# Kernel tuning notes

Measured on AMD Instinct MI355X. Metric: run time of the kernel, lower is better.

Reference implementation:

```python
import jax, jax.numpy as jnp
import numpy as np

B, H, S = 64, 1024, 512
MIN_VAL, MAX_VAL = -1.0, 1.0
EPS = 1e-8  # torch F.cosine_similarity default eps


def setup_inputs() -> dict:
    key = jax.random.key(0)
    k1, k2, k3 = jax.random.split(key, 3)
    tree_state = jax.random.normal(k1, (B, H), dtype=jnp.float32)
    seq_states = jax.random.normal(k2, (B, H, S), dtype=jnp.float32)
    # binary validity mask (float, as it is multiplied in)
    seq_mask = (jax.random.uniform(k3, (B, S)) < 0.9).astype(jnp.float32)
    return {"tree_state": tree_state, "seq_states": seq_states, "seq_mask": seq_mask}


def reference(tree_state, seq_states, seq_mask):
    # scan over the seq axis; carry h: (B, H)
    xs = (jnp.transpose(seq_states, (2, 0, 1)), seq_mask.T)  # (S,B,H), (S,B)

    def step(h, x):
        s, m = x  # s: (B,H), m: (B,)
        dot = jnp.sum(h * s, axis=-1)  # (B,)
        denom = jnp.maximum(
            jnp.linalg.norm(h, axis=-1) * jnp.linalg.norm(s, axis=-1), EPS
        )
        cos = (dot / denom)[:, None]  # (B,1)
        h_new = jnp.clip(h + (s - h * cos) * m[:, None], MIN_VAL, MAX_VAL)
        return h_new, None

    h, _ = jax.lax.scan(step, tree_state, xs)
    return h
```

## Files before the change

### kernel.cpp

```cpp
#include <hip/hip_runtime.h>


#define NB 64
#define NH 1024
#define NS 512

typedef float v4f __attribute__((ext_vector_type(4)));
typedef float v2f __attribute__((ext_vector_type(2)));

template <int N> struct ic { static constexpr int value = N; };

template <int CTRL>
__device__ __forceinline__ float dpp_add(float x) {
  int s = __builtin_amdgcn_update_dpp(0, __builtin_bit_cast(int, x), CTRL, 0xf,
                                      0xf, true);
  return x + __builtin_bit_cast(float, s);
}

__device__ __forceinline__ float readlane_f(float v, int lane) {
  return __builtin_bit_cast(
      float, __builtin_amdgcn_readlane(__builtin_bit_cast(int, v), lane));
}

__device__ __forceinline__ void wave_red3(float& a, float& b, float& c) {
  a = dpp_add<0x111>(a); b = dpp_add<0x111>(b); c = dpp_add<0x111>(c);
  a = dpp_add<0x112>(a); b = dpp_add<0x112>(b); c = dpp_add<0x112>(c);
  a = dpp_add<0x114>(a); b = dpp_add<0x114>(b); c = dpp_add<0x114>(c);
  a = dpp_add<0x118>(a); b = dpp_add<0x118>(b); c = dpp_add<0x118>(c);
  a = dpp_add<0x142>(a); b = dpp_add<0x142>(b); c = dpp_add<0x142>(c);
  a = dpp_add<0x143>(a); b = dpp_add<0x143>(b); c = dpp_add<0x143>(c);
  a = readlane_f(a, 63);
  b = readlane_f(b, 63);
  c = readlane_f(c, 63);
}

#define GLD4(dst, p) \
  asm volatile("global_load_dwordx4 %0, %1, off" : "=v"(dst) : "v"(p))
#define GLD1(dst, p) \
  asm volatile("global_load_dword %0, %1, off" : "=v"(dst) : "v"(p))

template <int IMM>
__device__ __forceinline__ void dsr128(v4f& d, unsigned a) {
  asm volatile("ds_read_b128 %[d], %[a] offset:%[o]"
               : [d] "=v"(d)
               : [a] "v"(a), [o] "n"(IMM));
}
template <int IMM>
__device__ __forceinline__ void dsw32(unsigned a, float v) {
  asm volatile("ds_write_b32 %[a], %[v] offset:%[o]" ::[a] "v"(a), [v] "v"(v),
               [o] "n"(IMM));
}

__device__ __forceinline__ v2f pk_fma(v2f a, v2f b, v2f c) {
  v2f d;
  asm("v_pk_fma_f32 %0, %1, %2, %3" : "=v"(d) : "v"(a), "v"(b), "v"(c));
  return d;
}
__device__ __forceinline__ v2f pk_mul(v2f a, v2f b) {
  v2f d;
  asm("v_pk_mul_f32 %0, %1, %2" : "=v"(d) : "v"(a), "v"(b));
  return d;
}
__device__ __forceinline__ v2f pk_add(v2f a, v2f b) {
  v2f d;
  asm("v_pk_add_f32 %0, %1, %2" : "=v"(d) : "v"(a), "v"(b));
  return d;
}

#define LGK0SV(s0, s1, s2, s3)                                       \
  asm volatile("s_waitcnt lgkmcnt(0)"                                \
               : "+v"(s0), "+v"(s1), "+v"(s2), "+v"(s3))

__global__ __launch_bounds__(256, 1) void otsu_scan_kernel(
    const float* __restrict__ tree,
    const float* __restrict__ seq,
    const float* __restrict__ mask,
    float* __restrict__ out) {
  __shared__ float lds[2 * 16 * 1024];
  const int b = blockIdx.x;
  const int tid = threadIdx.x;
  const int w = tid >> 6;
  const int l = tid & 63;
  const unsigned lb = (unsigned)(unsigned long long)(&lds[0]);

  if (w == 0) {
    const float* hrow = tree + b * NH + 4 * l;
    v4f hv0, hv1, hv2, hv3;
    GLD4(hv0, hrow);
    asm volatile("global_load_dwordx4 %0, %1, off offset:1024"
                 : "=v"(hv1) : "v"(hrow));
    asm volatile("global_load_dwordx4 %0, %1, off offset:2048"
                 : "=v"(hv2) : "v"(hrow));
    asm volatile("global_load_dwordx4 %0, %1, off offset:3072"
                 : "=v"(hv3) : "v"(hrow));
    float m8[8];
    {
      const float* mp = mask + b * NS + l;
      GLD1(m8[0], mp);
      GLD1(m8[1], mp + 64);
      GLD1(m8[2], mp + 128);
      GLD1(m8[3], mp + 192);
      GLD1(m8[4], mp + 256);
      GLD1(m8[5], mp + 320);
      GLD1(m8[6], mp + 384);
      GLD1(m8[7], mp + 448);
    }
    asm volatile("s_waitcnt vmcnt(0)"
                 : "+v"(hv0), "+v"(hv1), "+v"(hv2), "+v"(hv3), "+v"(m8[0]),
                   "+v"(m8[1]), "+v"(m8[2]), "+v"(m8[3]), "+v"(m8[4]),
                   "+v"(m8[5]), "+v"(m8[6]), "+v"(m8[7]));

    v2f h2[8];
    h2[0] = v2f{hv0[0], hv0[1]}; h2[1] = v2f{hv0[2], hv0[3]};
    h2[2] = v2f{hv1[0], hv1[1]}; h2[3] = v2f{hv1[2], hv1[3]};
    h2[4] = v2f{hv2[0], hv2[1]}; h2[5] = v2f{hv2[2], hv2[3]};
    h2[6] = v2f{hv3[0], hv3[1]}; h2[7] = v2f{hv3[2], hv3[3]};

    unsigned mbits = 0u;
#pragma unroll
    for (int i = 0; i < 8; ++i)
      if (m8[i] != 0.0f) mbits |= (1u << i);

    if (!(__builtin_amdgcn_readlane((int)mbits, 0) & 1)) {
#pragma unroll
      for (int p = 0; p < 8; ++p) {
        h2[p].x = __builtin_amdgcn_fmed3f(h2[p].x, -1.0f, 1.0f);
        h2[p].y = __builtin_amdgcn_fmed3f(h2[p].y, -1.0f, 1.0f);
      }
    }

    unsigned rb = lb + 16u * (unsigned)l;
    v4f sval[2][4];

    asm volatile("s_barrier" ::: "memory");

#pragma unroll 1
    for (int g = 0; g < 32; ++g) {
      const int lbase = (16 * g) & 63;
      const int msh = g >> 2;
      dsr128<0 * 4096 + 0>(sval[0][0], rb);
      dsr128<0 * 4096 + 1024>(sval[0][1], rb);
      dsr128<0 * 4096 + 2048>(sval[0][2], rb);
      dsr128<0 * 4096 + 3072>(sval[0][3], rb);
      auto step = [&](auto sc) {
        constexpr int T = decltype(sc)::value;
        LGK0SV(sval[T & 1][0], sval[T & 1][1], sval[T & 1][2],
               sval[T & 1][3]);
        if constexpr (T < 15) {
          dsr128<(T + 1) * 4096 + 0>(sval[(T + 1) & 1][0], rb);
          dsr128<(T + 1) * 4096 + 1024>(sval[(T + 1) & 1][1], rb);
          dsr128<(T + 1) * 4096 + 2048>(sval[(T + 1) & 1][2], rb);
          dsr128<(T + 1) * 4096 + 3072>(sval[(T + 1) & 1][3], rb);
        }
        const unsigned mw =
            (unsigned)__builtin_amdgcn_readlane((int)mbits, lbase + T);
        if ((mw >> msh) & 1u) {
          const v4f s0 = sval[T & 1][0], s1 = sval[T & 1][1],
                    s2 = sval[T & 1][2], s3 = sval[T & 1][3];
          v2f sp[8];
          sp[0] = v2f{s0[0], s0[1]}; sp[1] = v2f{s0[2], s0[3]};
          sp[2] = v2f{s1[0], s1[1]}; sp[3] = v2f{s1[2], s1[3]};
          sp[4] = v2f{s2[0], s2[1]}; sp[5] = v2f{s2[2], s2[3]};
          sp[6] = v2f{s3[0], s3[1]}; sp[7] = v2f{s3[2], s3[3]};
          v2f a0 = pk_mul(h2[0], sp[0]), a1 = pk_mul(h2[1], sp[1]);
          v2f a2 = pk_mul(h2[2], sp[2]), a3 = pk_mul(h2[3], sp[3]);
          v2f b0 = pk_mul(h2[0], h2[0]), b1 = pk_mul(h2[1], h2[1]);
          v2f b2 = pk_mul(h2[2], h2[2]), b3 = pk_mul(h2[3], h2[3]);
          v2f c0 = pk_mul(sp[0], sp[0]), c1 = pk_mul(sp[1], sp[1]);
          v2f c2 = pk_mul(sp[2], sp[2]), c3 = pk_mul(sp[3], sp[3]);
          a0 = pk_fma(h2[4], sp[4], a0); a1 = pk_fma(h2[5], sp[5], a1);
          a2 = pk_fma(h2[6], sp[6], a2); a3 = pk_fma(h2[7], sp[7], a3);
          b0 = pk_fma(h2[4], h2[4], b0); b1 = pk_fma(h2[5], h2[5], b1);
          b2 = pk_fma(h2[6], h2[6], b2); b3 = pk_fma(h2[7], h2[7], b3);
          c0 = pk_fma(sp[4], sp[4], c0); c1 = pk_fma(sp[5], sp[5], c1);
          c2 = pk_fma(sp[6], sp[6], c2); c3 = pk_fma(sp[7], sp[7], c3);
          v2f A = pk_add(pk_add(a0, a1), pk_add(a2, a3));
          v2f Bv = pk_add(pk_add(b0, b1), pk_add(b2, b3));
          v2f C = pk_add(pk_add(c0, c1), pk_add(c2, c3));
          float pd = A.x + A.y, ph = Bv.x + Bv.y, ps = C.x + C.y;
          wave_red3(pd, ph, ps);
          const float p = fmaxf(ph * ps, 1e-16f);
          const float cc = pd * __builtin_amdgcn_rsqf(p);
          const float aa = 1.0f - cc;
          const v2f av = v2f{aa, aa};
#pragma unroll
          for (int q = 0; q < 8; ++q) {
            v2f t = pk_fma(h2[q], av, sp[q]);
            h2[q].x = __builtin_amdgcn_fmed3f(t.x, -1.0f, 1.0f);
            h2[q].y = __builtin_amdgcn_fmed3f(t.y, -1.0f, 1.0f);
          }
        }
      };
      step(ic<0>{});  step(ic<1>{});  step(ic<2>{});  step(ic<3>{});
      step(ic<4>{});  step(ic<5>{});  step(ic<6>{});  step(ic<7>{});
      step(ic<8>{});  step(ic<9>{});  step(ic<10>{}); step(ic<11>{});
      step(ic<12>{}); step(ic<13>{}); step(ic<14>{}); step(ic<15>{});
      rb ^= 0x10000u;
      asm volatile("s_barrier" ::: "memory");
    }

    asm volatile("s_waitcnt vmcnt(0) lgkmcnt(0)" ::: "memory");
    float* orow = out + b * NH + 4 * l;
#pragma unroll
    for (int m = 0; m < 4; ++m) {
      float4 v;
      v.x = h2[2 * m].x;
      v.y = h2[2 * m].y;
      v.z = h2[2 * m + 1].x;
      v.w = h2[2 * m + 1].y;
      *(float4*)(orow + 256 * m) = v;
    }
  } else {
    const float* pbase = seq + (size_t)b * NH * NS + (l >> 2) * 512 +
                         (l & 3) * 4;
    const unsigned wpb =
        lb + 16384u * (unsigned)(l & 3) + 4u * (unsigned)(l >> 2);
    const int cb = w - 1;

    v4f ring[22];
#define STAGE(T_, BSEL_)                                                  \
    do {                                                                  \
      _Pragma("unroll") for (int k = 0; k < 22; ++k) {                    \
        const int c = 3 * k + cb;                                         \
        if (c < 64) {                                                     \
          const float* p_ = pbase + c * 8192 + (T_) * 16;                 \
          GLD4(ring[k], p_);                                              \
        }                                                                 \
      }                                                                   \
      asm volatile("s_waitcnt vmcnt(0)" ::: "memory");                    \
      _Pragma("unroll") for (int k = 0; k < 22; ++k) {                    \
        const int c = 3 * k + cb;                                         \
        if (c < 64) {                                                     \
          const unsigned a_ = wpb + (BSEL_) + 64u * (unsigned)c;          \
          dsw32<0>(a_, ring[k][0]);                                       \
          dsw32<4096>(a_, ring[k][1]);                                    \
          dsw32<8192>(a_, ring[k][2]);                                    \
          dsw32<12288>(a_, ring[k][3]);                                   \
        }                                                                 \
      }                                                                   \
      asm volatile("s_waitcnt lgkmcnt(0)" ::: "memory");                  \
    } while (0)

    STAGE(0, 0u);
    asm volatile("s_barrier" ::: "memory");

#pragma unroll 1
    for (int g = 0; g < 32; ++g) {
      if (g < 31) {
        const unsigned bsel = (unsigned)((g + 1) & 1) << 16;
        STAGE(g + 1, bsel);
      }
      asm volatile("s_barrier" ::: "memory");
    }
#undef STAGE
  }
}

extern "C" void kernel_launch(void* const* d_in, const int* in_sizes, int n_in,
                              void* d_out, int out_size, void* d_ws,
                              size_t ws_size, hipStream_t stream) {
  const float* tree = (const float*)d_in[0];
  const float* seq = (const float*)d_in[1];
  const float* mask = (const float*)d_in[2];
  float* out = (float*)d_out;
  otsu_scan_kernel<<<dim3(NB), dim3(256), 0, stream>>>(tree, seq, mask, out);
}
```

Before: 270.4 us.

## Pad LDS rows and deepen consumer LDS read prefetch to two steps

Pads each time-step row in LDS from 1024 to 1028 floats so the producer waves' strided 32-bit writes no longer all hit the same banks. The consumer wave now keeps three register buffers and issues LDS reads two steps ahead, waiting with lgkmcnt(4) instead of draining to zero. This hides more of the LDS read latency behind the serial per-step dot/norm/update chain. In exchange it uses more VGPRs and slightly more LDS, and relies on a finer-grained wait count being correct.

```diff
diff --git a/kernel.cpp b/kernel.cpp
--- a/kernel.cpp
+++ b/kernel.cpp
@@ -4,6 +4,9 @@
 #define NB 64
 #define NH 1024
 #define NS 512
+
+#define STRF 1028
+#define BUFF (16 * STRF)
 
 typedef float v4f __attribute__((ext_vector_type(4)));
 typedef float v2f __attribute__((ext_vector_type(2)));
@@ -67,16 +70,21 @@
   return d;
 }
 
-#define LGK0SV(s0, s1, s2, s3)                                       \
-  asm volatile("s_waitcnt lgkmcnt(0)"                                \
-               : "+v"(s0), "+v"(s1), "+v"(s2), "+v"(s3))
+#define LGK4SV(sv)                                                    \
+  asm volatile("s_waitcnt lgkmcnt(4)"                                 \
+               : "+v"((sv)[0]), "+v"((sv)[1]), "+v"((sv)[2]),         \
+                 "+v"((sv)[3]))
+#define LGK0SV(sv)                                                    \
+  asm volatile("s_waitcnt lgkmcnt(0)"                                 \
+               : "+v"((sv)[0]), "+v"((sv)[1]), "+v"((sv)[2]),         \
+                 "+v"((sv)[3]))
 
 __global__ __launch_bounds__(256, 1) void otsu_scan_kernel(
     const float* __restrict__ tree,
     const float* __restrict__ seq,
     const float* __restrict__ mask,
     float* __restrict__ out) {
-  __shared__ float lds[2 * 16 * 1024];
+  __shared__ float lds[2 * BUFF];
   const int b = blockIdx.x;
   const int tid = threadIdx.x;
   const int w = tid >> 6;
@@ -129,8 +137,8 @@
       }
     }
 
-    unsigned rb = lb + 16u * (unsigned)l;
-    v4f sval[2][4];
+    const unsigned rb0 = lb + 16u * (unsigned)l;
+    v4f sval[3][4];
 
     asm volatile("s_barrier" ::: "memory");
 
@@ -138,25 +146,33 @@
     for (int g = 0; g < 32; ++g) {
       const int lbase = (16 * g) & 63;
       const int msh = g >> 2;
-      dsr128<0 * 4096 + 0>(sval[0][0], rb);
-      dsr128<0 * 4096 + 1024>(sval[0][1], rb);
-      dsr128<0 * 4096 + 2048>(sval[0][2], rb);
-      dsr128<0 * 4096 + 3072>(sval[0][3], rb);
+      const unsigned rbuf = rb0 + ((g & 1) ? (unsigned)(BUFF * 4) : 0u);
+
+      dsr128<0 * 4112 + 0>(sval[0][0], rbuf);
+      dsr128<0 * 4112 + 1024>(sval[0][1], rbuf);
+      dsr128<0 * 4112 + 2048>(sval[0][2], rbuf);
+      dsr128<0 * 4112 + 3072>(sval[0][3], rbuf);
+      dsr128<1 * 4112 + 0>(sval[1][0], rbuf);
+      dsr128<1 * 4112 + 1024>(sval[1][1], rbuf);
+      dsr128<1 * 4112 + 2048>(sval[1][2], rbuf);
+      dsr128<1 * 4112 + 3072>(sval[1][3], rbuf);
+      LGK4SV(sval[0]);
+
       auto step = [&](auto sc) {
         constexpr int T = decltype(sc)::value;
-        LGK0SV(sval[T & 1][0], sval[T & 1][1], sval[T & 1][2],
-               sval[T & 1][3]);
-        if constexpr (T < 15) {
-          dsr128<(T + 1) * 4096 + 0>(sval[(T + 1) & 1][0], rb);
-          dsr128<(T + 1) * 4096 + 1024>(sval[(T + 1) & 1][1], rb);
-          dsr128<(T + 1) * 4096 + 2048>(sval[(T + 1) & 1][2], rb);
-          dsr128<(T + 1) * 4096 + 3072>(sval[(T + 1) & 1][3], rb);
+        if constexpr (T >= 1 && T <= 14) LGK4SV(sval[T % 3]);
+        else if constexpr (T == 15) LGK0SV(sval[0]);
+        if constexpr (T <= 13) {
+          dsr128<(T + 2) * 4112 + 0>(sval[(T + 2) % 3][0], rbuf);
+          dsr128<(T + 2) * 4112 + 1024>(sval[(T + 2) % 3][1], rbuf);
+          dsr128<(T + 2) * 4112 + 2048>(sval[(T + 2) % 3][2], rbuf);
+          dsr128<(T + 2) * 4112 + 3072>(sval[(T + 2) % 3][3], rbuf);
         }
         const unsigned mw =
             (unsigned)__builtin_amdgcn_readlane((int)mbits, lbase + T);
         if ((mw >> msh) & 1u) {
-          const v4f s0 = sval[T & 1][0], s1 = sval[T & 1][1],
-                    s2 = sval[T & 1][2], s3 = sval[T & 1][3];
+          const v4f s0 = sval[T % 3][0], s1 = sval[T % 3][1],
+                    s2 = sval[T % 3][2], s3 = sval[T % 3][3];
           v2f sp[8];
           sp[0] = v2f{s0[0], s0[1]}; sp[1] = v2f{s0[2], s0[3]};
           sp[2] = v2f{s1[0], s1[1]}; sp[3] = v2f{s1[2], s1[3]};
@@ -195,7 +211,6 @@
       step(ic<4>{});  step(ic<5>{});  step(ic<6>{});  step(ic<7>{});
       step(ic<8>{});  step(ic<9>{});  step(ic<10>{}); step(ic<11>{});
       step(ic<12>{}); step(ic<13>{}); step(ic<14>{}); step(ic<15>{});
-      rb ^= 0x10000u;
       asm volatile("s_barrier" ::: "memory");
     }
 
@@ -214,7 +229,7 @@
     const float* pbase = seq + (size_t)b * NH * NS + (l >> 2) * 512 +
                          (l & 3) * 4;
     const unsigned wpb =
-        lb + 16384u * (unsigned)(l & 3) + 4u * (unsigned)(l >> 2);
+        lb + 16448u * (unsigned)(l & 3) + 4u * (unsigned)(l >> 2);
     const int cb = w - 1;
 
     v4f ring[22];
@@ -232,10 +247,10 @@
         const int c = 3 * k + cb;                                         \
         if (c < 64) {                                                     \
           const unsigned a_ = wpb + (BSEL_) + 64u * (unsigned)c;          \
-          dsw32<0>(a_, ring[k][0]);                                       \
-          dsw32<4096>(a_, ring[k][1]);                                    \
-          dsw32<8192>(a_, ring[k][2]);                                    \
-          dsw32<12288>(a_, ring[k][3]);                                   \
+          dsw32<0 * 4112>(a_, ring[k][0]);                                \
+          dsw32<1 * 4112>(a_, ring[k][1]);                                \
+          dsw32<2 * 4112>(a_, ring[k][2]);                                \
+          dsw32<3 * 4112>(a_, ring[k][3]);                                \
         }                                                                 \
       }                                                                   \
       asm volatile("s_waitcnt lgkmcnt(0)" ::: "memory");                  \
@@ -247,7 +262,7 @@
 #pragma unroll 1
     for (int g = 0; g < 32; ++g) {
       if (g < 31) {
-        const unsigned bsel = (unsigned)((g + 1) & 1) << 16;
+        const unsigned bsel = ((g + 1) & 1) ? (unsigned)(BUFF * 4) : 0u;
         STAGE(g + 1, bsel);
       }
       asm volatile("s_barrier" ::: "memory");
```

New measurement: 266.0 us. About the same (-1.6%).

## Process two batch rows per block to interleave independent scan chains

Applied to the files above, without the earlier changes.

Each block now handles two batch rows with 32 blocks instead of 64. The compute wave runs both recurrences side by side, merging their wave reductions into one six-value DPP reduction, so one chain's latency can hide behind the other's. The LDS stage is re-laid out with a padded stride of 4112 bytes, which changes bank mapping, and holds 8 steps per stage over 64 rounds instead of 16 steps over 32. The cost is half as many CUs in use, twice the load traffic per block, and compute that is no longer skipped for masked steps.

```diff
diff --git a/kernel.cpp b/kernel.cpp
--- a/kernel.cpp
+++ b/kernel.cpp
@@ -1,9 +1,12 @@
 #include <hip/hip_runtime.h>
 
 
-#define NB 64
+#define NB 32
 #define NH 1024
 #define NS 512
+
+#define STRB 4112u
+#define BUFB 32896u
 
 typedef float v4f __attribute__((ext_vector_type(4)));
 typedef float v2f __attribute__((ext_vector_type(2)));
@@ -22,20 +25,29 @@
       float, __builtin_amdgcn_readlane(__builtin_bit_cast(int, v), lane));
 }
 
-__device__ __forceinline__ void wave_red3(float& a, float& b, float& c) {
+__device__ __forceinline__ void wave_red6(float& a, float& b, float& c,
+                                          float& d, float& e, float& f) {
   a = dpp_add<0x111>(a); b = dpp_add<0x111>(b); c = dpp_add<0x111>(c);
+  d = dpp_add<0x111>(d); e = dpp_add<0x111>(e); f = dpp_add<0x111>(f);
   a = dpp_add<0x112>(a); b = dpp_add<0x112>(b); c = dpp_add<0x112>(c);
+  d = dpp_add<0x112>(d); e = dpp_add<0x112>(e); f = dpp_add<0x112>(f);
   a = dpp_add<0x114>(a); b = dpp_add<0x114>(b); c = dpp_add<0x114>(c);
+  d = dpp_add<0x114>(d); e = dpp_add<0x114>(e); f = dpp_add<0x114>(f);
   a = dpp_add<0x118>(a); b = dpp_add<0x118>(b); c = dpp_add<0x118>(c);
+  d = dpp_add<0x118>(d); e = dpp_add<0x118>(e); f = dpp_add<0x118>(f);
   a = dpp_add<0x142>(a); b = dpp_add<0x142>(b); c = dpp_add<0x142>(c);
+  d = dpp_add<0x142>(d); e = dpp_add<0x142>(e); f = dpp_add<0x142>(f);
   a = dpp_add<0x143>(a); b = dpp_add<0x143>(b); c = dpp_add<0x143>(c);
-  a = readlane_f(a, 63);
-  b = readlane_f(b, 63);
-  c = readlane_f(c, 63);
+  d = dpp_add<0x143>(d); e = dpp_add<0x143>(e); f = dpp_add<0x143>(f);
+  a = readlane_f(a, 63); b = readlane_f(b, 63); c = readlane_f(c, 63);
+  d = readlane_f(d, 63); e = readlane_f(e, 63); f = readlane_f(f, 63);
 }
 
 #define GLD4(dst, p) \
   asm volatile("global_load_dwordx4 %0, %1, off" : "=v"(dst) : "v"(p))
+#define GLD4O(dst, p, OFF) \
+  asm volatile("global_load_dwordx4 %0, %1, off offset:" OFF \
+               : "=v"(dst) : "v"(p))
 #define GLD1(dst, p) \
   asm volatile("global_load_dword %0, %1, off" : "=v"(dst) : "v"(p))
 
@@ -67,188 +79,261 @@
   return d;
 }
 
-#define LGK0SV(s0, s1, s2, s3)                                       \
-  asm volatile("s_waitcnt lgkmcnt(0)"                                \
-               : "+v"(s0), "+v"(s1), "+v"(s2), "+v"(s3))
+template <int T>
+__device__ __forceinline__ void read_step(unsigned rb, v4f (&sv)[4]) {
+  dsr128<(int)(T * STRB) + 0>(sv[0], rb);
+  dsr128<(int)(T * STRB) + 1024>(sv[1], rb);
+  dsr128<(int)(T * STRB) + 2048>(sv[2], rb);
+  dsr128<(int)(T * STRB) + 3072>(sv[3], rb);
+}
+
+#define LGK0AB(a, b)                                                   \
+  asm volatile("s_waitcnt lgkmcnt(0)"                                  \
+               : "+v"((a)[0]), "+v"((a)[1]), "+v"((a)[2]),             \
+                 "+v"((a)[3]), "+v"((b)[0]), "+v"((b)[1]),             \
+                 "+v"((b)[2]), "+v"((b)[3]))
 
 __global__ __launch_bounds__(256, 1) void otsu_scan_kernel(
     const float* __restrict__ tree,
     const float* __restrict__ seq,
     const float* __restrict__ mask,
     float* __restrict__ out) {
-  __shared__ float lds[2 * 16 * 1024];
-  const int b = blockIdx.x;
+  __shared__ float lds[4 * 8 * 1028];
   const int tid = threadIdx.x;
   const int w = tid >> 6;
   const int l = tid & 63;
+  const int bA = 2 * blockIdx.x;
+  const int bB = bA + 1;
   const unsigned lb = (unsigned)(unsigned long long)(&lds[0]);
 
   if (w == 0) {
-    const float* hrow = tree + b * NH + 4 * l;
-    v4f hv0, hv1, hv2, hv3;
-    GLD4(hv0, hrow);
-    asm volatile("global_load_dwordx4 %0, %1, off offset:1024"
-                 : "=v"(hv1) : "v"(hrow));
-    asm volatile("global_load_dwordx4 %0, %1, off offset:2048"
-                 : "=v"(hv2) : "v"(hrow));
-    asm volatile("global_load_dwordx4 %0, %1, off offset:3072"
-                 : "=v"(hv3) : "v"(hrow));
-    float m8[8];
+    const float* hrA = tree + bA * NH + 4 * l;
+    const float* hrB = tree + bB * NH + 4 * l;
+    v4f hA0, hA1, hA2v, hA3, hB0, hB1, hB2v, hB3;
+    GLD4(hA0, hrA);
+    GLD4O(hA1, hrA, "1024");
+    GLD4O(hA2v, hrA, "2048");
+    GLD4O(hA3, hrA, "3072");
+    GLD4(hB0, hrB);
+    GLD4O(hB1, hrB, "1024");
+    GLD4O(hB2v, hrB, "2048");
+    GLD4O(hB3, hrB, "3072");
+    float mA[8], mB[8];
     {
-      const float* mp = mask + b * NS + l;
-      GLD1(m8[0], mp);
-      GLD1(m8[1], mp + 64);
-      GLD1(m8[2], mp + 128);
-      GLD1(m8[3], mp + 192);
-      GLD1(m8[4], mp + 256);
-      GLD1(m8[5], mp + 320);
-      GLD1(m8[6], mp + 384);
-      GLD1(m8[7], mp + 448);
+      const float* mpA = mask + bA * NS + l;
+      const float* mpB = mask + bB * NS + l;
+#pragma unroll
+      for (int i = 0; i < 8; ++i) GLD1(mA[i], mpA + 64 * i);
+#pragma unroll
+      for (int i = 0; i < 8; ++i) GLD1(mB[i], mpB + 64 * i);
     }
     asm volatile("s_waitcnt vmcnt(0)"
-                 : "+v"(hv0), "+v"(hv1), "+v"(hv2), "+v"(hv3), "+v"(m8[0]),
-                   "+v"(m8[1]), "+v"(m8[2]), "+v"(m8[3]), "+v"(m8[4]),
-                   "+v"(m8[5]), "+v"(m8[6]), "+v"(m8[7]));
-
-    v2f h2[8];
-    h2[0] = v2f{hv0[0], hv0[1]}; h2[1] = v2f{hv0[2], hv0[3]};
-    h2[2] = v2f{hv1[0], hv1[1]}; h2[3] = v2f{hv1[2], hv1[3]};
-    h2[4] = v2f{hv2[0], hv2[1]}; h2[5] = v2f{hv2[2], hv2[3]};
-    h2[6] = v2f{hv3[0], hv3[1]}; h2[7] = v2f{hv3[2], hv3[3]};
-
-    unsigned mbits = 0u;
-#pragma unroll
-    for (int i = 0; i < 8; ++i)
-      if (m8[i] != 0.0f) mbits |= (1u << i);
-
-    if (!(__builtin_amdgcn_readlane((int)mbits, 0) & 1)) {
+                 : "+v"(hA0), "+v"(hA1), "+v"(hA2v), "+v"(hA3), "+v"(hB0),
+                   "+v"(hB1), "+v"(hB2v), "+v"(hB3));
+    asm volatile("s_waitcnt vmcnt(0)"
+                 : "+v"(mA[0]), "+v"(mA[1]), "+v"(mA[2]), "+v"(mA[3]),
+                   "+v"(mA[4]), "+v"(mA[5]), "+v"(mA[6]), "+v"(mA[7]),
+                   "+v"(mB[0]), "+v"(mB[1]), "+v"(mB[2]), "+v"(mB[3]),
+                   "+v"(mB[4]), "+v"(mB[5]), "+v"(mB[6]), "+v"(mB[7]));
+
+    v2f hA[8], hB[8];
+    hA[0] = v2f{hA0[0], hA0[1]}; hA[1] = v2f{hA0[2], hA0[3]};
+    hA[2] = v2f{hA1[0], hA1[1]}; hA[3] = v2f{hA1[2], hA1[3]};
+    hA[4] = v2f{hA2v[0], hA2v[1]}; hA[5] = v2f{hA2v[2], hA2v[3]};
+    hA[6] = v2f{hA3[0], hA3[1]}; hA[7] = v2f{hA3[2], hA3[3]};
+    hB[0] = v2f{hB0[0], hB0[1]}; hB[1] = v2f{hB0[2], hB0[3]};
+    hB[2] = v2f{hB1[0], hB1[1]}; hB[3] = v2f{hB1[2], hB1[3]};
+    hB[4] = v2f{hB2v[0], hB2v[1]}; hB[5] = v2f{hB2v[2], hB2v[3]};
+    hB[6] = v2f{hB3[0], hB3[1]}; hB[7] = v2f{hB3[2], hB3[3]};
+
+    unsigned mbitsA = 0u, mbitsB = 0u;
+#pragma unroll
+    for (int i = 0; i < 8; ++i) {
+      if (mA[i] != 0.0f) mbitsA |= (1u << i);
+      if (mB[i] != 0.0f) mbitsB |= (1u << i);
+    }
+
+    if (!(__builtin_amdgcn_readlane((int)mbitsA, 0) & 1)) {
 #pragma unroll
       for (int p = 0; p < 8; ++p) {
-        h2[p].x = __builtin_amdgcn_fmed3f(h2[p].x, -1.0f, 1.0f);
-        h2[p].y = __builtin_amdgcn_fmed3f(h2[p].y, -1.0f, 1.0f);
+        hA[p].x = __builtin_amdgcn_fmed3f(hA[p].x, -1.0f, 1.0f);
+        hA[p].y = __builtin_amdgcn_fmed3f(hA[p].y, -1.0f, 1.0f);
       }
     }
-
-    unsigned rb = lb + 16u * (unsigned)l;
-    v4f sval[2][4];
+    if (!(__builtin_amdgcn_readlane((int)mbitsB, 0) & 1)) {
+#pragma unroll
+      for (int p = 0; p < 8; ++p) {
+        hB[p].x = __builtin_amdgcn_fmed3f(hB[p].x, -1.0f, 1.0f);
+        hB[p].y = __builtin_amdgcn_fmed3f(hB[p].y, -1.0f, 1.0f);
+      }
+    }
+
+    const unsigned rbA0 = lb + 16u * (unsigned)l;
+    const unsigned rbB0 = rbA0 + 2u * BUFB;
+    v4f svA[2][4], svB[2][4];
 
     asm volatile("s_barrier" ::: "memory");
 
 #pragma unroll 1
-    for (int g = 0; g < 32; ++g) {
-      const int lbase = (16 * g) & 63;
-      const int msh = g >> 2;
-      dsr128<0 * 4096 + 0>(sval[0][0], rb);
-      dsr128<0 * 4096 + 1024>(sval[0][1], rb);
-      dsr128<0 * 4096 + 2048>(sval[0][2], rb);
-      dsr128<0 * 4096 + 3072>(sval[0][3], rb);
+    for (int g = 0; g < 64; ++g) {
+      const int lbase = 8 * (g & 7);
+      const int msh = g >> 3;
+      const unsigned po = (g & 1) ? BUFB : 0u;
+      const unsigned rbA = rbA0 + po;
+      const unsigned rbB = rbB0 + po;
+
+      read_step<0>(rbA, svA[0]);
+      read_step<0>(rbB, svB[0]);
+
       auto step = [&](auto sc) {
         constexpr int T = decltype(sc)::value;
-        LGK0SV(sval[T & 1][0], sval[T & 1][1], sval[T & 1][2],
-               sval[T & 1][3]);
-        if constexpr (T < 15) {
-          dsr128<(T + 1) * 4096 + 0>(sval[(T + 1) & 1][0], rb);
-          dsr128<(T + 1) * 4096 + 1024>(sval[(T + 1) & 1][1], rb);
-          dsr128<(T + 1) * 4096 + 2048>(sval[(T + 1) & 1][2], rb);
-          dsr128<(T + 1) * 4096 + 3072>(sval[(T + 1) & 1][3], rb);
+        LGK0AB(svA[T & 1], svB[T & 1]);
+        if constexpr (T < 7) {
+          read_step<T + 1>(rbA, svA[(T + 1) & 1]);
+          read_step<T + 1>(rbB, svB[(T + 1) & 1]);
         }
-        const unsigned mw =
-            (unsigned)__builtin_amdgcn_readlane((int)mbits, lbase + T);
-        if ((mw >> msh) & 1u) {
-          const v4f s0 = sval[T & 1][0], s1 = sval[T & 1][1],
-                    s2 = sval[T & 1][2], s3 = sval[T & 1][3];
-          v2f sp[8];
-          sp[0] = v2f{s0[0], s0[1]}; sp[1] = v2f{s0[2], s0[3]};
-          sp[2] = v2f{s1[0], s1[1]}; sp[3] = v2f{s1[2], s1[3]};
-          sp[4] = v2f{s2[0], s2[1]}; sp[5] = v2f{s2[2], s2[3]};
-          sp[6] = v2f{s3[0], s3[1]}; sp[7] = v2f{s3[2], s3[3]};
-          v2f a0 = pk_mul(h2[0], sp[0]), a1 = pk_mul(h2[1], sp[1]);
-          v2f a2 = pk_mul(h2[2], sp[2]), a3 = pk_mul(h2[3], sp[3]);
-          v2f b0 = pk_mul(h2[0], h2[0]), b1 = pk_mul(h2[1], h2[1]);
-          v2f b2 = pk_mul(h2[2], h2[2]), b3 = pk_mul(h2[3], h2[3]);
-          v2f c0 = pk_mul(sp[0], sp[0]), c1 = pk_mul(sp[1], sp[1]);
-          v2f c2 = pk_mul(sp[2], sp[2]), c3 = pk_mul(sp[3], sp[3]);
-          a0 = pk_fma(h2[4], sp[4], a0); a1 = pk_fma(h2[5], sp[5], a1);
-          a2 = pk_fma(h2[6], sp[6], a2); a3 = pk_fma(h2[7], sp[7], a3);
-          b0 = pk_fma(h2[4], h2[4], b0); b1 = pk_fma(h2[5], h2[5], b1);
-          b2 = pk_fma(h2[6], h2[6], b2); b3 = pk_fma(h2[7], h2[7], b3);
-          c0 = pk_fma(sp[4], sp[4], c0); c1 = pk_fma(sp[5], sp[5], c1);
-          c2 = pk_fma(sp[6], sp[6], c2); c3 = pk_fma(sp[7], sp[7], c3);
-          v2f A = pk_add(pk_add(a0, a1), pk_add(a2, a3));
-          v2f Bv = pk_add(pk_add(b0, b1), pk_add(b2, b3));
-          v2f C = pk_add(pk_add(c0, c1), pk_add(c2, c3));
-          float pd = A.x + A.y, ph = Bv.x + Bv.y, ps = C.x + C.y;
-          wave_red3(pd, ph, ps);
-          const float p = fmaxf(ph * ps, 1e-16f);
-          const float cc = pd * __builtin_amdgcn_rsqf(p);
-          const float aa = 1.0f - cc;
-          const v2f av = v2f{aa, aa};
+        const v4f a0 = svA[T & 1][0], a1 = svA[T & 1][1],
+                  a2 = svA[T & 1][2], a3 = svA[T & 1][3];
+        const v4f b0 = svB[T & 1][0], b1 = svB[T & 1][1],
+                  b2 = svB[T & 1][2], b3 = svB[T & 1][3];
+        v2f sa[8], sb[8];
+        sa[0] = v2f{a0[0], a0[1]}; sa[1] = v2f{a0[2], a0[3]};
+        sa[2] = v2f{a1[0], a1[1]}; sa[3] = v2f{a1[2], a1[3]};
+        sa[4] = v2f{a2[0], a2[1]}; sa[5] = v2f{a2[2], a2[3]};
+        sa[6] = v2f{a3[0], a3[1]}; sa[7] = v2f{a3[2], a3[3]};
+        sb[0] = v2f{b0[0], b0[1]}; sb[1] = v2f{b0[2], b0[3]};
+        sb[2] = v2f{b1[0], b1[1]}; sb[3] = v2f{b1[2], b1[3]};
+        sb[4] = v2f{b2[0], b2[1]}; sb[5] = v2f{b2[2], b2[3]};
+        sb[6] = v2f{b3[0], b3[1]}; sb[7] = v2f{b3[2], b3[3]};
+        v2f dA0 = pk_mul(hA[0], sa[0]), dB0 = pk_mul(hB[0], sb[0]);
+        v2f dA1 = pk_mul(hA[1], sa[1]), dB1 = pk_mul(hB[1], sb[1]);
+        v2f dA2 = pk_mul(hA[2], sa[2]), dB2 = pk_mul(hB[2], sb[2]);
+        v2f dA3 = pk_mul(hA[3], sa[3]), dB3 = pk_mul(hB[3], sb[3]);
+        v2f eA0 = pk_mul(hA[0], hA[0]), eB0 = pk_mul(hB[0], hB[0]);
+        v2f eA1 = pk_mul(hA[1], hA[1]), eB1 = pk_mul(hB[1], hB[1]);
+        v2f eA2 = pk_mul(hA[2], hA[2]), eB2 = pk_mul(hB[2], hB[2]);
+        v2f eA3 = pk_mul(hA[3], hA[3]), eB3 = pk_mul(hB[3], hB[3]);
+        v2f fA0 = pk_mul(sa[0], sa[0]), fB0 = pk_mul(sb[0], sb[0]);
+        v2f fA1 = pk_mul(sa[1], sa[1]), fB1 = pk_mul(sb[1], sb[1]);
+        v2f fA2 = pk_mul(sa[2], sa[2]), fB2 = pk_mul(sb[2], sb[2]);
+        v2f fA3 = pk_mul(sa[3], sa[3]), fB3 = pk_mul(sb[3], sb[3]);
+        dA0 = pk_fma(hA[4], sa[4], dA0); dB0 = pk_fma(hB[4], sb[4], dB0);
+        dA1 = pk_fma(hA[5], sa[5], dA1); dB1 = pk_fma(hB[5], sb[5], dB1);
+        dA2 = pk_fma(hA[6], sa[6], dA2); dB2 = pk_fma(hB[6], sb[6], dB2);
+        dA3 = pk_fma(hA[7], sa[7], dA3); dB3 = pk_fma(hB[7], sb[7], dB3);
+        eA0 = pk_fma(hA[4], hA[4], eA0); eB0 = pk_fma(hB[4], hB[4], eB0);
+        eA1 = pk_fma(hA[5], hA[5], eA1); eB1 = pk_fma(hB[5], hB[5], eB1);
+        eA2 = pk_fma(hA[6], hA[6], eA2); eB2 = pk_fma(hB[6], hB[6], eB2);
+        eA3 = pk_fma(hA[7], hA[7], eA3); eB3 = pk_fma(hB[7], hB[7], eB3);
+        fA0 = pk_fma(sa[4], sa[4], fA0); fB0 = pk_fma(sb[4], sb[4], fB0);
+        fA1 = pk_fma(sa[5], sa[5], fA1); fB1 = pk_fma(sb[5], sb[5], fB1);
+        fA2 = pk_fma(sa[6], sa[6], fA2); fB2 = pk_fma(sb[6], sb[6], fB2);
+        fA3 = pk_fma(sa[7], sa[7], fA3); fB3 = pk_fma(sb[7], sb[7], fB3);
+        v2f DA = pk_add(pk_add(dA0, dA1), pk_add(dA2, dA3));
+        v2f DB = pk_add(pk_add(dB0, dB1), pk_add(dB2, dB3));
+        v2f EA = pk_add(pk_add(eA0, eA1), pk_add(eA2, eA3));
+        v2f EB = pk_add(pk_add(eB0, eB1), pk_add(eB2, eB3));
+        v2f FA = pk_add(pk_add(fA0, fA1), pk_add(fA2, fA3));
+        v2f FB = pk_add(pk_add(fB0, fB1), pk_add(fB2, fB3));
+        float pdA = DA.x + DA.y, phA = EA.x + EA.y, psA = FA.x + FA.y;
+        float pdB = DB.x + DB.y, phB = EB.x + EB.y, psB = FB.x + FB.y;
+        wave_red6(pdA, phA, psA, pdB, phB, psB);
+        const float qA = fmaxf(phA * psA, 1e-16f);
+        const float qB = fmaxf(phB * psB, 1e-16f);
+        const float cA = pdA * __builtin_amdgcn_rsqf(qA);
+        const float cB = pdB * __builtin_amdgcn_rsqf(qB);
+        const float aaA = 1.0f - cA;
+        const float aaB = 1.0f - cB;
+        const unsigned mwA =
+            (unsigned)__builtin_amdgcn_readlane((int)mbitsA, lbase + T);
+        const unsigned mwB =
+            (unsigned)__builtin_amdgcn_readlane((int)mbitsB, lbase + T);
+        if ((mwA >> msh) & 1u) {
+          const v2f av = v2f{aaA, aaA};
 #pragma unroll
           for (int q = 0; q < 8; ++q) {
-            v2f t = pk_fma(h2[q], av, sp[q]);
-            h2[q].x = __builtin_amdgcn_fmed3f(t.x, -1.0f, 1.0f);
-            h2[q].y = __builtin_amdgcn_fmed3f(t.y, -1.0f, 1.0f);
+            v2f t = pk_fma(hA[q], av, sa[q]);
+            hA[q].x = __builtin_amdgcn_fmed3f(t.x, -1.0f, 1.0f);
+            hA[q].y = __builtin_amdgcn_fmed3f(t.y, -1.0f, 1.0f);
+          }
+        }
+        if ((mwB >> msh) & 1u) {
+          const v2f av = v2f{aaB, aaB};
+#pragma unroll
+          for (int q = 0; q < 8; ++q) {
+            v2f t = pk_fma(hB[q], av, sb[q]);
+            hB[q].x = __builtin_amdgcn_fmed3f(t.x, -1.0f, 1.0f);
+            hB[q].y = __builtin_amdgcn_fmed3f(t.y, -1.0f, 1.0f);
           }
         }
       };
-      step(ic<0>{});  step(ic<1>{});  step(ic<2>{});  step(ic<3>{});
-      step(ic<4>{});  step(ic<5>{});  step(ic<6>{});  step(ic<7>{});
-      step(ic<8>{});  step(ic<9>{});  step(ic<10>{}); step(ic<11>{});
-      step(ic<12>{}); step(ic<13>{}); step(ic<14>{}); step(ic<15>{});
-      rb ^= 0x10000u;
+      step(ic<0>{}); step(ic<1>{}); step(ic<2>{}); step(ic<3>{});
+      step(ic<4>{}); step(ic<5>{}); step(ic<6>{}); step(ic<7>{});
       asm volatile("s_barrier" ::: "memory");
     }
 
     asm volatile("s_waitcnt vmcnt(0) lgkmcnt(0)" ::: "memory");
-    float* orow = out + b * NH + 4 * l;
+    float* orA = out + bA * NH + 4 * l;
+    float* orB = out + bB * NH + 4 * l;
 #pragma unroll
     for (int m = 0; m < 4; ++m) {
       float4 v;
-      v.x = h2[2 * m].x;
-      v.y = h2[2 * m].y;
-      v.z = h2[2 * m + 1].x;
-      v.w = h2[2 * m + 1].y;
-      *(float4*)(orow + 256 * m) = v;
+      v.x = hA[2 * m].x; v.y = hA[2 * m].y;
+      v.z = hA[2 * m + 1].x; v.w = hA[2 * m + 1].y;
+      *(float4*)(orA + 256 * m) = v;
+    }
+#pragma unroll
+    for (int m = 0; m < 4; ++m) {
+      float4 v;
+      v.x = hB[2 * m].x; v.y = hB[2 * m].y;
+      v.z = hB[2 * m + 1].x; v.w = hB[2 * m + 1].y;
+      *(float4*)(orB + 256 * m) = v;
     }
   } else {
-    const float* pbase = seq + (size_t)b * NH * NS + (l >> 2) * 512 +
-                         (l & 3) * 4;
-    const unsigned wpb =
-        lb + 16384u * (unsigned)(l & 3) + 4u * (unsigned)(l >> 2);
+    const float* pbA = seq + (size_t)bA * NH * NS + (l >> 1) * 512 +
+                       (l & 1) * 4;
+    const float* pbB = seq + (size_t)bB * NH * NS + (l >> 1) * 512 +
+                       (l & 1) * 4;
+    const unsigned wbase =
+        lb + 16448u * (unsigned)(l & 1) + 4u * (unsigned)(l >> 1);
     const int cb = w - 1;
 
     v4f ring[22];
-#define STAGE(T_, BSEL_)                                                  \
+#define STAGE(T_)                                                         \
     do {                                                                  \
+      const int to_ = 8 * (T_);                                           \
+      const unsigned po_ = ((T_) & 1) ? BUFB : 0u;                        \
       _Pragma("unroll") for (int k = 0; k < 22; ++k) {                    \
-        const int c = 3 * k + cb;                                         \
-        if (c < 64) {                                                     \
-          const float* p_ = pbase + c * 8192 + (T_) * 16;                 \
+        const int cc = 3 * k + cb;                                        \
+        if (cc < 64) {                                                    \
+          const float* p_ = ((cc < 32) ? (pbA + cc * 16384)               \
+                                       : (pbB + (cc - 32) * 16384)) +     \
+                            to_;                                          \
           GLD4(ring[k], p_);                                              \
         }                                                                 \
       }                                                                   \
       asm volatile("s_waitcnt vmcnt(0)" ::: "memory");                    \
       _Pragma("unroll") for (int k = 0; k < 22; ++k) {                    \
-        const int c = 3 * k + cb;                                         \
-        if (c < 64) {                                                     \
-          const unsigned a_ = wpb + (BSEL_) + 64u * (unsigned)c;          \
-          dsw32<0>(a_, ring[k][0]);                                       \
-          dsw32<4096>(a_, ring[k][1]);                                    \
-          dsw32<8192>(a_, ring[k][2]);                                    \
-          dsw32<12288>(a_, ring[k][3]);                                   \
+        const int cc = 3 * k + cb;                                        \
+        if (cc < 64) {                                                    \
+          const unsigned a_ = wbase + po_ +                               \
+              ((cc < 32) ? 0u : 2u * BUFB) + 128u * (unsigned)(cc & 31);  \
+          dsw32<0 * 4112>(a_, ring[k][0]);                                \
+          dsw32<1 * 4112>(a_, ring[k][1]);                                \
+          dsw32<2 * 4112>(a_, ring[k][2]);                                \
+          dsw32<3 * 4112>(a_, ring[k][3]);                                \
         }                                                                 \
       }                                                                   \
       asm volatile("s_waitcnt lgkmcnt(0)" ::: "memory");                  \
     } while (0)
 
-    STAGE(0, 0u);
+    STAGE(0);
     asm volatile("s_barrier" ::: "memory");
 
 #pragma unroll 1
-    for (int g = 0; g < 32; ++g) {
-      if (g < 31) {
-        const unsigned bsel = (unsigned)((g + 1) & 1) << 16;
-        STAGE(g + 1, bsel);
+    for (int g = 0; g < 64; ++g) {
+      if (g < 63) {
+        STAGE(g + 1);
       }
       asm volatile("s_barrier" ::: "memory");
     }
```

Result: slower. 403.0 us (+49.0%).
